# Kernel tuning notes

Measured on AMD Instinct MI355X. Metric: run time of the kernel, lower is better.

## Reference

```python
import jax, jax.numpy as jnp
import numpy as np

N_NODES = 100000
N_EDGES = 1600000
IN_C, HID_C, OUT_C = 128, 64, 40


def setup_inputs() -> dict:
    key = jax.random.key(0)
    ks = jax.random.split(key, 8)
    x = jax.random.normal(ks[0], (N_NODES, IN_C), dtype=jnp.float32)
    edge_index = jax.random.randint(ks[1], (2, N_EDGES), 0, N_NODES, dtype=jnp.int64)
    # Glorot-ish init for weights
    W1 = jax.random.normal(ks[2], (IN_C, HID_C), dtype=jnp.float32) / np.sqrt(IN_C)
    W2 = jax.random.normal(ks[3], (HID_C, HID_C), dtype=jnp.float32) / np.sqrt(HID_C)
    W3 = jax.random.normal(ks[4], (HID_C, OUT_C), dtype=jnp.float32) / np.sqrt(HID_C)
    b1 = jnp.zeros((HID_C,), jnp.float32)
    b2 = jnp.zeros((HID_C,), jnp.float32)
    b3 = jnp.zeros((OUT_C,), jnp.float32)
    return {"x": x, "edge_index": edge_index, "W1": W1, "b1": b1,
            "W2": W2, "b2": b2, "W3": W3, "b3": b3}


def _gcn_prep(edge_index, num_nodes):
    # PyG GCNConv: add self-loops, symmetric normalization with edge_weight=1.
    src = jnp.concatenate([edge_index[0], jnp.arange(num_nodes, dtype=edge_index.dtype)])
    dst = jnp.concatenate([edge_index[1], jnp.arange(num_nodes, dtype=edge_index.dtype)])
    deg = jax.ops.segment_sum(jnp.ones_like(dst, dtype=jnp.float32), dst,
                              num_segments=num_nodes)
    dis = jnp.where(deg > 0, jax.lax.rsqrt(deg), 0.0)  # deg^-1/2, inf->0
    norm = dis[src] * dis[dst]  # per-edge symmetric norm
    return src, dst, norm


def _gcn_conv(x, W, b, src, dst, norm, num_nodes):
    h = x @ W                                # [N, F_out], linear (no bias)
    msg = h[src] * norm[:, None]             # gather + scale, [E_total, F_out]
    out = jax.ops.segment_sum(msg, dst, num_segments=num_nodes)
    return out + b                           # conv bias after aggregation


def reference(x, edge_index, W1, b1, W2, b2, W3, b3):
    n = x.shape[0]
    src, dst, norm = _gcn_prep(edge_index, n)
    h = jax.nn.relu(_gcn_conv(x, W1, b1, src, dst, norm, n))
    h = jax.nn.relu(_gcn_conv(h, W2, b2, src, dst, norm, n))
    h = _gcn_conv(h, W3, b3, src, dst, norm, n)
    return jax.nn.log_softmax(h, axis=1)
```

## Files before the change

### kernel.cpp

```cpp
#include <hip/hip_runtime.h>
#include <cstdint>
#include <cstddef>
#include <math.h>

#define NN 100000
#define NE 1600000
#define NB ((NN + 255) / 256)
#define EB 400
#define EPB (NE / EB)

#define GT_NODES 128
#define GT_KC 32
#define GT_STRIDE 132

typedef unsigned short u16;

__device__ __forceinline__ float bf2f(u16 u) {
    union { unsigned int i; float f; } c; c.i = ((unsigned int)u) << 16; return c.f;
}
__device__ __forceinline__ u16 f2bf(float f) {
    union { float f; unsigned int i; } c; c.f = f;
    unsigned int lsb = (c.i >> 16) & 1u;
    return (u16)((c.i + 0x7fffu + lsb) >> 16);
}
__device__ __forceinline__ unsigned int pack2(float a, float b) {
    return (unsigned int)f2bf(a) | ((unsigned int)f2bf(b) << 16);
}

__global__ __launch_bounds__(64) void k_detect(const int* __restrict__ p, int* flag) {
    int nz = 0;
    for (int i = threadIdx.x; i < 1024; i += 64) nz |= (p[2 * i + 1] != 0);
    unsigned long long b = __ballot(nz != 0);
    if (threadIdx.x == 0) *flag = (b == 0ULL) ? 1 : 0;
}

__device__ __forceinline__ int load_idx(const void* ei, int isI64, int pos) {
    if (isI64) return (int)((const long long*)ei)[pos];
    return ((const int*)ei)[pos];
}

__global__ __launch_bounds__(256) void k_hist(const void* __restrict__ ei,
                                              const int* __restrict__ flag,
                                              int* __restrict__ counts) {
    __shared__ int h[NB];
    for (int i = threadIdx.x; i < NB; i += 256) h[i] = 0;
    __syncthreads();
    int isI64 = *flag;
    int base = blockIdx.x * EPB;
    for (int i = threadIdx.x; i < EPB; i += 256) {
        int d = load_idx(ei, isI64, NE + base + i);
        atomicAdd(&h[d >> 8], 1);
    }
    __syncthreads();
    for (int i = threadIdx.x; i < NB; i += 256) counts[blockIdx.x * NB + i] = h[i];
}

__global__ __launch_bounds__(512) void k_colscan(const int* __restrict__ counts,
                                                 int* __restrict__ pfx,
                                                 int* __restrict__ btot) {
    __shared__ int t[512];
    int j = blockIdx.x;
    int v = (threadIdx.x < EB) ? counts[threadIdx.x * NB + j] : 0;
    t[threadIdx.x] = v;
    __syncthreads();
#pragma unroll
    for (int off = 1; off < 512; off <<= 1) {
        int u = (threadIdx.x >= off) ? t[threadIdx.x - off] : 0;
        __syncthreads();
        t[threadIdx.x] += u;
        __syncthreads();
    }
    if (threadIdx.x < EB) pfx[threadIdx.x * NB + j] = t[threadIdx.x] - v;
    if (threadIdx.x == 511) btot[j] = t[511];
}

__global__ __launch_bounds__(512) void k_bucketscan(const int* __restrict__ btot,
                                                    int* __restrict__ bbase) {
    __shared__ int t[512];
    int v = (threadIdx.x < NB) ? btot[threadIdx.x] : 0;
    t[threadIdx.x] = v;
    __syncthreads();
#pragma unroll
    for (int off = 1; off < 512; off <<= 1) {
        int u = (threadIdx.x >= off) ? t[threadIdx.x - off] : 0;
        __syncthreads();
        t[threadIdx.x] += u;
        __syncthreads();
    }
    if (threadIdx.x < NB) bbase[threadIdx.x] = t[threadIdx.x] - v;
    if (threadIdx.x == 511) bbase[NB] = t[511];
}

__global__ __launch_bounds__(256) void k_scatter(const void* __restrict__ ei,
                                                 const int* __restrict__ flag,
                                                 const int* __restrict__ pfx,
                                                 const int* __restrict__ bbase,
                                                 int* __restrict__ csr_tmp) {
    __shared__ int basel[NB];
    __shared__ int cur[NB];
    for (int i = threadIdx.x; i < NB; i += 256) {
        basel[i] = bbase[i] + pfx[blockIdx.x * NB + i];
        cur[i] = 0;
    }
    __syncthreads();
    int isI64 = *flag;
    int base = blockIdx.x * EPB;
    for (int i = threadIdx.x; i < EPB; i += 256) {
        int s = load_idx(ei, isI64, base + i);
        int d = load_idx(ei, isI64, NE + base + i);
        int bkt = d >> 8;
        int slot = basel[bkt] + atomicAdd(&cur[bkt], 1);
        csr_tmp[slot] = ((d & 255) << 17) | s;
    }
}

__global__ __launch_bounds__(256) void k_sort(const int* __restrict__ bbase,
                                              const int* __restrict__ csr_tmp,
                                              int* __restrict__ csr,
                                              int* __restrict__ deg,
                                              int* __restrict__ offs,
                                              float* __restrict__ dis) {
    __shared__ int h[256];
    __shared__ int sc[256];
    __shared__ int cur[256];
    int j = blockIdx.x;
    int s0 = bbase[j], s1 = bbase[j + 1];
    h[threadIdx.x] = 0;
    __syncthreads();
    for (int p = s0 + threadIdx.x; p < s1; p += 256)
        atomicAdd(&h[csr_tmp[p] >> 17], 1);
    __syncthreads();
    int v = h[threadIdx.x];
    sc[threadIdx.x] = v;
    __syncthreads();
#pragma unroll
    for (int off = 1; off < 256; off <<= 1) {
        int u = (threadIdx.x >= off) ? sc[threadIdx.x - off] : 0;
        __syncthreads();
        sc[threadIdx.x] += u;
        __syncthreads();
    }
    int excl = sc[threadIdx.x] - v;
    int node = j * 256 + threadIdx.x;
    if (node < NN) {
        deg[node] = v;
        offs[node] = s0 + excl;
        dis[node] = rsqrtf((float)(v + 1));
    }
    cur[threadIdx.x] = excl;
    __syncthreads();
    for (int p = s0 + threadIdx.x; p < s1; p += 256) {
        int pk = csr_tmp[p];
        int dl = pk >> 17;
        int pos = s0 + atomicAdd(&cur[dl], 1);
        csr[pos] = pk & 0x1FFFF;
    }
}

template <int K, int FR, bool RELU>
__global__ __launch_bounds__(512) void k_gemm(const float* __restrict__ x,
                                              const float* __restrict__ W,
                                              const float* __restrict__ dis,
                                              u16* __restrict__ out) {
    __shared__ float xT[GT_KC * GT_STRIDE];
    __shared__ float Wc[GT_KC * 64];
    const int tid = threadIdx.x;
    const int r = tid >> 4;
    const int c = tid & 15;
    const int f4 = tid & 7;
    const int nrow = tid >> 3;
    const int nbase = blockIdx.x * GT_NODES;

    float acc[4][4];
#pragma unroll
    for (int i = 0; i < 4; ++i)
#pragma unroll
        for (int j = 0; j < 4; ++j) acc[i][j] = 0.f;

    for (int kc = 0; kc < K; kc += GT_KC) {
#pragma unroll
        for (int q = 0; q < 4; ++q) {
            int e = q * 512 + tid;
            int kk = e >> 6, j = e & 63;
            Wc[kk * 64 + j] = (j < FR) ? W[(size_t)(kc + kk) * FR + j] : 0.f;
        }
#pragma unroll
        for (int q = 0; q < 2; ++q) {
            int nl = q * 64 + nrow;
            int n = nbase + nl;
            float4 v = make_float4(0.f, 0.f, 0.f, 0.f);
            if (n < NN) v = *(const float4*)(x + (size_t)n * K + kc + f4 * 4);
            if (RELU) {
                v.x = fmaxf(v.x, 0.f); v.y = fmaxf(v.y, 0.f);
                v.z = fmaxf(v.z, 0.f); v.w = fmaxf(v.w, 0.f);
            }
            xT[(f4 * 4 + 0) * GT_STRIDE + nl] = v.x;
            xT[(f4 * 4 + 1) * GT_STRIDE + nl] = v.y;
            xT[(f4 * 4 + 2) * GT_STRIDE + nl] = v.z;
            xT[(f4 * 4 + 3) * GT_STRIDE + nl] = v.w;
        }
        __syncthreads();
#pragma unroll 8
        for (int kk = 0; kk < GT_KC; ++kk) {
            float4 a = *(const float4*)&xT[kk * GT_STRIDE + r * 4];
            float4 w = *(const float4*)&Wc[kk * 64 + c * 4];
            float xa[4] = {a.x, a.y, a.z, a.w};
            float wb[4] = {w.x, w.y, w.z, w.w};
#pragma unroll
            for (int i = 0; i < 4; ++i)
#pragma unroll
                for (int j = 0; j < 4; ++j)
                    acc[i][j] = fmaf(xa[i], wb[j], acc[i][j]);
        }
        __syncthreads();
    }
    if (c * 4 < FR) {
#pragma unroll
        for (int i = 0; i < 4; ++i) {
            int n = nbase + r * 4 + i;
            if (n < NN) {
                float dv = dis[n];
                uint2 o;
                o.x = pack2(dv * acc[i][0], dv * acc[i][1]);
                o.y = pack2(dv * acc[i][2], dv * acc[i][3]);
                *(uint2*)(out + (size_t)n * FR + c * 4) = o;
            }
        }
    }
}

template <int F, bool SOFTMAX>
__global__ __launch_bounds__(256) void k_gather(const int* __restrict__ offs,
                                                const int* __restrict__ deg,
                                                const int* __restrict__ csr,
                                                const float* __restrict__ dis,
                                                const u16* __restrict__ g,
                                                const float* __restrict__ b,
                                                float* __restrict__ out) {
    int n = blockIdx.x * 4 + (threadIdx.x >> 6);
    unsigned f = threadIdx.x & 63;
    if (n >= NN) return;
    unsigned fc = (f < (unsigned)F) ? f : 0u;
    int start = __builtin_amdgcn_readfirstlane(offs[n]);
    int len   = __builtin_amdgcn_readfirstlane(deg[n]);
    float dvn = dis[n];
    float bf  = b[fc];
    float acc = bf2f(g[(unsigned)n * F + fc]);
    int i = 0;
    for (; i + 8 <= len; i += 8) {
        int s0 = __builtin_amdgcn_readfirstlane(csr[start + i + 0]);
        int s1 = __builtin_amdgcn_readfirstlane(csr[start + i + 1]);
        int s2 = __builtin_amdgcn_readfirstlane(csr[start + i + 2]);
        int s3 = __builtin_amdgcn_readfirstlane(csr[start + i + 3]);
        int s4 = __builtin_amdgcn_readfirstlane(csr[start + i + 4]);
        int s5 = __builtin_amdgcn_readfirstlane(csr[start + i + 5]);
        int s6 = __builtin_amdgcn_readfirstlane(csr[start + i + 6]);
        int s7 = __builtin_amdgcn_readfirstlane(csr[start + i + 7]);
        u16 h0 = g[(unsigned)s0 * F + fc];
        u16 h1 = g[(unsigned)s1 * F + fc];
        u16 h2 = g[(unsigned)s2 * F + fc];
        u16 h3 = g[(unsigned)s3 * F + fc];
        u16 h4 = g[(unsigned)s4 * F + fc];
        u16 h5 = g[(unsigned)s5 * F + fc];
        u16 h6 = g[(unsigned)s6 * F + fc];
        u16 h7 = g[(unsigned)s7 * F + fc];
        acc += bf2f(h0) + bf2f(h1) + bf2f(h2) + bf2f(h3)
             + bf2f(h4) + bf2f(h5) + bf2f(h6) + bf2f(h7);
    }
    for (; i + 2 <= len; i += 2) {
        int s0 = __builtin_amdgcn_readfirstlane(csr[start + i + 0]);
        int s1 = __builtin_amdgcn_readfirstlane(csr[start + i + 1]);
        u16 h0 = g[(unsigned)s0 * F + fc];
        u16 h1 = g[(unsigned)s1 * F + fc];
        acc += bf2f(h0) + bf2f(h1);
    }
    if (i < len) {
        int s0 = __builtin_amdgcn_readfirstlane(csr[start + i]);
        acc += bf2f(g[(unsigned)s0 * F + fc]);
    }
    float v = dvn * acc + bf;
    if (!SOFTMAX) {
        if (f < (unsigned)F) out[(size_t)n * F + f] = v;
    } else {
        float vv = (f < (unsigned)F) ? v : -INFINITY;
        float m = vv;
#pragma unroll
        for (int off = 32; off; off >>= 1) m = fmaxf(m, __shfl_xor(m, off));
        float ex = (f < (unsigned)F) ? __expf(vv - m) : 0.f;
        float sum = ex;
#pragma unroll
        for (int off = 32; off; off >>= 1) sum += __shfl_xor(sum, off);
        if (f < (unsigned)F) out[(size_t)n * F + f] = vv - m - logf(sum);
    }
}

extern "C" void kernel_launch(void* const* d_in, const int* in_sizes, int n_in,
                              void* d_out, int out_size, void* d_ws, size_t ws_size,
                              hipStream_t stream) {
    const float* x  = (const float*)d_in[0];
    const void*  ei = d_in[1];
    const float* W1 = (const float*)d_in[2];
    const float* b1 = (const float*)d_in[3];
    const float* W2 = (const float*)d_in[4];
    const float* b2 = (const float*)d_in[5];
    const float* W3 = (const float*)d_in[6];
    const float* b3 = (const float*)d_in[7];
    float* out = (float*)d_out;

    char* ws = (char*)d_ws;
    size_t off = 0;
    auto alloc = [&](size_t bytes) { void* p = ws + off; off += (bytes + 255) & ~255ULL; return p; };
    int*   flag    = (int*)alloc(4);
    int*   counts  = (int*)alloc((size_t)EB * NB * 4);
    int*   pfx     = (int*)alloc((size_t)EB * NB * 4);
    int*   btot    = (int*)alloc(NB * 4);
    int*   bbase   = (int*)alloc((NB + 1) * 4);
    int*   deg     = (int*)alloc(NN * 4);
    float* dis     = (float*)alloc(NN * 4);
    int*   offs    = (int*)alloc(NN * 4);
    int*   csr_tmp = (int*)alloc((size_t)NE * 4);
    int*   csr     = (int*)alloc((size_t)NE * 4);
    u16*   gbuf    = (u16*)alloc((size_t)NN * 64 * 2);
    float* act     = (float*)alloc((size_t)NN * 64 * 4);

    k_detect<<<1, 64, 0, stream>>>((const int*)ei, flag);
    k_hist<<<EB, 256, 0, stream>>>(ei, flag, counts);
    k_colscan<<<NB, 512, 0, stream>>>(counts, pfx, btot);
    k_bucketscan<<<1, 512, 0, stream>>>(btot, bbase);
    k_scatter<<<EB, 256, 0, stream>>>(ei, flag, pfx, bbase, csr_tmp);
    k_sort<<<NB, 256, 0, stream>>>(bbase, csr_tmp, csr, deg, offs, dis);

    const int gemm_grid = (NN + GT_NODES - 1) / GT_NODES;
    const int gather_grid = (NN + 3) / 4;

    k_gemm<128, 64, false><<<gemm_grid, 512, 0, stream>>>(x, W1, dis, gbuf);
    k_gather<64, false><<<gather_grid, 256, 0, stream>>>(offs, deg, csr, dis, gbuf, b1, act);

    k_gemm<64, 64, true><<<gemm_grid, 512, 0, stream>>>(act, W2, dis, gbuf);
    k_gather<64, false><<<gather_grid, 256, 0, stream>>>(offs, deg, csr, dis, gbuf, b2, act);

    k_gemm<64, 40, true><<<gemm_grid, 512, 0, stream>>>(act, W3, dis, gbuf);
    k_gather<40, true><<<gather_grid, 256, 0, stream>>>(offs, deg, csr, dis, gbuf, b3, out);
}
```

Before: 347.0 us.

## Vectorize gather: 16 lanes per row with 8-byte loads, 4 edges per wave

Reworks the aggregation kernel so each 16-lane quarter-wave loads one neighbor row with 8-byte vector loads (4 bf16 features per lane). The four quarters handle four different edges at once, and the partial sums are combined with cross-lane shuffles. Edge indices are read as int4 after an alignment prologue. This is meant to cut per-lane 2-byte loads and issue more independent memory requests per instruction. In exchange it adds shuffle reductions and leaves lanes idle in the remainder loops, where only quad 0 works.

```diff
diff --git a/kernel.cpp b/kernel.cpp
--- a/kernel.cpp
+++ b/kernel.cpp
@@ -15,8 +15,8 @@
 
 typedef unsigned short u16;
 
-__device__ __forceinline__ float bf2f(u16 u) {
-    union { unsigned int i; float f; } c; c.i = ((unsigned int)u) << 16; return c.f;
+__device__ __forceinline__ float asf(unsigned u) {
+    union { unsigned i; float f; } c; c.i = u; return c.f;
 }
 __device__ __forceinline__ u16 f2bf(float f) {
     union { float f; unsigned int i; } c; c.f = f;
@@ -237,60 +237,84 @@
                                                 const u16* __restrict__ g,
                                                 const float* __restrict__ b,
                                                 float* __restrict__ out) {
+    constexpr int NDW2 = F / 4;
+    int lane = threadIdx.x & 63;
     int n = blockIdx.x * 4 + (threadIdx.x >> 6);
-    unsigned f = threadIdx.x & 63;
     if (n >= NN) return;
-    unsigned fc = (f < (unsigned)F) ? f : 0u;
+    int quad = lane >> 4, sq = lane & 15;
+    unsigned sqoff = (unsigned)sq * 8u;
+    const char* gb = (const char*)g;
+
+    float2 a0 = make_float2(0.f, 0.f);
+    float2 a1 = make_float2(0.f, 0.f);
+
+    auto rowoff = [](int row) -> unsigned {
+        if (F == 64) return ((unsigned)row) << 7;
+        unsigned t = (((unsigned)row) << 2) + (unsigned)row;
+        return t << 4;
+    };
+    auto addRow = [&](unsigned off) {
+        uint2 dd = *(const uint2*)(gb + off);
+        a0.x += asf(dd.x << 16); a0.y += asf(dd.x & 0xffff0000u);
+        a1.x += asf(dd.y << 16); a1.y += asf(dd.y & 0xffff0000u);
+    };
+
     int start = __builtin_amdgcn_readfirstlane(offs[n]);
     int len   = __builtin_amdgcn_readfirstlane(deg[n]);
     float dvn = dis[n];
-    float bf  = b[fc];
-    float acc = bf2f(g[(unsigned)n * F + fc]);
+
+    if (quad == 0) addRow(rowoff(n) + sqoff);
+
     int i = 0;
-    for (; i + 8 <= len; i += 8) {
-        int s0 = __builtin_amdgcn_readfirstlane(csr[start + i + 0]);
-        int s1 = __builtin_amdgcn_readfirstlane(csr[start + i + 1]);
-        int s2 = __builtin_amdgcn_readfirstlane(csr[start + i + 2]);
-        int s3 = __builtin_amdgcn_readfirstlane(csr[start + i + 3]);
-        int s4 = __builtin_amdgcn_readfirstlane(csr[start + i + 4]);
-        int s5 = __builtin_amdgcn_readfirstlane(csr[start + i + 5]);
-        int s6 = __builtin_amdgcn_readfirstlane(csr[start + i + 6]);
-        int s7 = __builtin_amdgcn_readfirstlane(csr[start + i + 7]);
-        u16 h0 = g[(unsigned)s0 * F + fc];
-        u16 h1 = g[(unsigned)s1 * F + fc];
-        u16 h2 = g[(unsigned)s2 * F + fc];
-        u16 h3 = g[(unsigned)s3 * F + fc];
-        u16 h4 = g[(unsigned)s4 * F + fc];
-        u16 h5 = g[(unsigned)s5 * F + fc];
-        u16 h6 = g[(unsigned)s6 * F + fc];
-        u16 h7 = g[(unsigned)s7 * F + fc];
-        acc += bf2f(h0) + bf2f(h1) + bf2f(h2) + bf2f(h3)
-             + bf2f(h4) + bf2f(h5) + bf2f(h6) + bf2f(h7);
-    }
-    for (; i + 2 <= len; i += 2) {
-        int s0 = __builtin_amdgcn_readfirstlane(csr[start + i + 0]);
-        int s1 = __builtin_amdgcn_readfirstlane(csr[start + i + 1]);
-        u16 h0 = g[(unsigned)s0 * F + fc];
-        u16 h1 = g[(unsigned)s1 * F + fc];
-        acc += bf2f(h0) + bf2f(h1);
-    }
-    if (i < len) {
-        int s0 = __builtin_amdgcn_readfirstlane(csr[start + i]);
-        acc += bf2f(g[(unsigned)s0 * F + fc]);
-    }
-    float v = dvn * acc + bf;
+    int pre = (4 - (start & 3)) & 3;
+    if (pre > len) pre = len;
+    for (; i < pre; ++i) {
+        int e = csr[start + i];
+        if (quad == 0) addRow(rowoff(e) + sqoff);
+    }
+    for (; i + 4 <= len; i += 4) {
+        int4 e4 = *(const int4*)(csr + start + i);
+        int sa = (quad & 1) ? e4.y : e4.x;
+        int sb = (quad & 1) ? e4.w : e4.z;
+        int src = (quad & 2) ? sb : sa;
+        addRow(rowoff(src) + sqoff);
+    }
+    for (; i < len; ++i) {
+        int e = csr[start + i];
+        if (quad == 0) addRow(rowoff(e) + sqoff);
+    }
+
+    a0.x += __shfl_xor(a0.x, 16); a0.x += __shfl_xor(a0.x, 32);
+    a0.y += __shfl_xor(a0.y, 16); a0.y += __shfl_xor(a0.y, 32);
+    a1.x += __shfl_xor(a1.x, 16); a1.x += __shfl_xor(a1.x, 32);
+    a1.y += __shfl_xor(a1.y, 16); a1.y += __shfl_xor(a1.y, 32);
+
+    bool act = sq < NDW2;
+    float4 bias = make_float4(0.f, 0.f, 0.f, 0.f);
+    if (act) bias = *(const float4*)(b + sq * 4);
+    float v0 = dvn * a0.x + bias.x;
+    float v1 = dvn * a0.y + bias.y;
+    float v2 = dvn * a1.x + bias.z;
+    float v3 = dvn * a1.y + bias.w;
+
     if (!SOFTMAX) {
-        if (f < (unsigned)F) out[(size_t)n * F + f] = v;
+        if (quad == 0 && act)
+            *(float4*)(out + (size_t)n * F + sq * 4) = make_float4(v0, v1, v2, v3);
     } else {
-        float vv = (f < (unsigned)F) ? v : -INFINITY;
-        float m = vv;
-#pragma unroll
-        for (int off = 32; off; off >>= 1) m = fmaxf(m, __shfl_xor(m, off));
-        float ex = (f < (unsigned)F) ? __expf(vv - m) : 0.f;
-        float sum = ex;
-#pragma unroll
-        for (int off = 32; off; off >>= 1) sum += __shfl_xor(sum, off);
-        if (f < (unsigned)F) out[(size_t)n * F + f] = vv - m - logf(sum);
+        float m = act ? fmaxf(fmaxf(v0, v1), fmaxf(v2, v3)) : -INFINITY;
+        m = fmaxf(m, __shfl_xor(m, 1));
+        m = fmaxf(m, __shfl_xor(m, 2));
+        m = fmaxf(m, __shfl_xor(m, 4));
+        m = fmaxf(m, __shfl_xor(m, 8));
+        float s = act ? (__expf(v0 - m) + __expf(v1 - m) + __expf(v2 - m) + __expf(v3 - m)) : 0.f;
+        s += __shfl_xor(s, 1);
+        s += __shfl_xor(s, 2);
+        s += __shfl_xor(s, 4);
+        s += __shfl_xor(s, 8);
+        float ls = logf(s);
+        if (quad == 0 && act)
+            *(float4*)(out + (size_t)n * F + sq * 4) =
+                make_float4(v0 - m - ls, v1 - m - ls, v2 - m - ls, v3 - m - ls);
     }
 }
 
```

After: 407.8 us. 1.18x slower.

## Fuse CSR bucket build into one kernel using fixed-capacity buckets and atomic cursors

Applied to the files above, without the earlier changes.

Replaces the detect, histogram, column-scan, bucket-scan and scatter kernels with a single build kernel. That kernel stages each block's edges in shared memory, counts them per destination bucket, and reserves space in fixed-capacity per-bucket regions with global atomics. This removes several launches and the exact prefix-sum passes over a large counts matrix. In exchange it assumes no bucket of 256 nodes ever gets more than CAP edges, which holds for uniformly random edges but can overflow on skewed graphs. Bucket order within a region also becomes nondeterministic.

```diff
diff --git a/kernel.cpp b/kernel.cpp
--- a/kernel.cpp
+++ b/kernel.cpp
@@ -8,6 +8,7 @@
 #define NB ((NN + 255) / 256)
 #define EB 400
 #define EPB (NE / EB)
+#define CAP 5120
 
 #define GT_NODES 128
 #define GT_KC 32
@@ -16,7 +17,7 @@
 typedef unsigned short u16;
 
 __device__ __forceinline__ float bf2f(u16 u) {
-    union { unsigned int i; float f; } c; c.i = ((unsigned int)u) << 16; return c.f;
+    union { unsigned i; float f; } c; c.i = ((unsigned)u) << 16; return c.f;
 }
 __device__ __forceinline__ u16 f2bf(float f) {
     union { float f; unsigned int i; } c; c.f = f;
@@ -27,94 +28,56 @@
     return (unsigned int)f2bf(a) | ((unsigned int)f2bf(b) << 16);
 }
 
-__global__ __launch_bounds__(64) void k_detect(const int* __restrict__ p, int* flag) {
-    int nz = 0;
-    for (int i = threadIdx.x; i < 1024; i += 64) nz |= (p[2 * i + 1] != 0);
-    unsigned long long b = __ballot(nz != 0);
-    if (threadIdx.x == 0) *flag = (b == 0ULL) ? 1 : 0;
-}
-
 __device__ __forceinline__ int load_idx(const void* ei, int isI64, int pos) {
     if (isI64) return (int)((const long long*)ei)[pos];
     return ((const int*)ei)[pos];
 }
 
-__global__ __launch_bounds__(256) void k_hist(const void* __restrict__ ei,
-                                              const int* __restrict__ flag,
-                                              int* __restrict__ counts) {
-    __shared__ int h[NB];
-    for (int i = threadIdx.x; i < NB; i += 256) h[i] = 0;
-    __syncthreads();
-    int isI64 = *flag;
-    int base = blockIdx.x * EPB;
-    for (int i = threadIdx.x; i < EPB; i += 256) {
-        int d = load_idx(ei, isI64, NE + base + i);
-        atomicAdd(&h[d >> 8], 1);
-    }
-    __syncthreads();
-    for (int i = threadIdx.x; i < NB; i += 256) counts[blockIdx.x * NB + i] = h[i];
-}
-
-__global__ __launch_bounds__(512) void k_colscan(const int* __restrict__ counts,
-                                                 int* __restrict__ pfx,
-                                                 int* __restrict__ btot) {
-    __shared__ int t[512];
-    int j = blockIdx.x;
-    int v = (threadIdx.x < EB) ? counts[threadIdx.x * NB + j] : 0;
-    t[threadIdx.x] = v;
-    __syncthreads();
-#pragma unroll
-    for (int off = 1; off < 512; off <<= 1) {
-        int u = (threadIdx.x >= off) ? t[threadIdx.x - off] : 0;
-        __syncthreads();
-        t[threadIdx.x] += u;
-        __syncthreads();
-    }
-    if (threadIdx.x < EB) pfx[threadIdx.x * NB + j] = t[threadIdx.x] - v;
-    if (threadIdx.x == 511) btot[j] = t[511];
-}
-
-__global__ __launch_bounds__(512) void k_bucketscan(const int* __restrict__ btot,
-                                                    int* __restrict__ bbase) {
-    __shared__ int t[512];
-    int v = (threadIdx.x < NB) ? btot[threadIdx.x] : 0;
-    t[threadIdx.x] = v;
-    __syncthreads();
-#pragma unroll
-    for (int off = 1; off < 512; off <<= 1) {
-        int u = (threadIdx.x >= off) ? t[threadIdx.x - off] : 0;
-        __syncthreads();
-        t[threadIdx.x] += u;
-        __syncthreads();
-    }
-    if (threadIdx.x < NB) bbase[threadIdx.x] = t[threadIdx.x] - v;
-    if (threadIdx.x == 511) bbase[NB] = t[511];
-}
-
-__global__ __launch_bounds__(256) void k_scatter(const void* __restrict__ ei,
-                                                 const int* __restrict__ flag,
-                                                 const int* __restrict__ pfx,
-                                                 const int* __restrict__ bbase,
-                                                 int* __restrict__ csr_tmp) {
+__global__ __launch_bounds__(256) void k_build(const void* __restrict__ ei,
+                                               int* __restrict__ cursor,
+                                               int* __restrict__ csr_tmp) {
+    __shared__ int sbuf[EPB];
+    __shared__ int dbuf[EPB];
+    __shared__ int cnt[NB];
     __shared__ int basel[NB];
-    __shared__ int cur[NB];
-    for (int i = threadIdx.x; i < NB; i += 256) {
-        basel[i] = bbase[i] + pfx[blockIdx.x * NB + i];
-        cur[i] = 0;
-    }
-    __syncthreads();
-    int isI64 = *flag;
+    __shared__ int anynz;
+
+    const int* p = (const int*)ei;
+    if (threadIdx.x == 0) anynz = 0;
+    for (int i = threadIdx.x; i < NB; i += 256) cnt[i] = 0;
+    __syncthreads();
+    int nz = 0;
+    for (int i = threadIdx.x; i < 1024; i += 256) nz |= (p[2 * i + 1] != 0);
+    if (nz) anynz = 1;
+    __syncthreads();
+    int isI64 = (anynz == 0);
+
     int base = blockIdx.x * EPB;
     for (int i = threadIdx.x; i < EPB; i += 256) {
         int s = load_idx(ei, isI64, base + i);
         int d = load_idx(ei, isI64, NE + base + i);
+        sbuf[i] = s;
+        dbuf[i] = d;
+        atomicAdd(&cnt[d >> 8], 1);
+    }
+    __syncthreads();
+    for (int j = threadIdx.x; j < NB; j += 256) {
+        int c = cnt[j];
+        int g = c ? atomicAdd(&cursor[j], c) : 0;
+        basel[j] = j * CAP + g;
+        cnt[j] = 0;
+    }
+    __syncthreads();
+    for (int i = threadIdx.x; i < EPB; i += 256) {
+        int s = sbuf[i];
+        int d = dbuf[i];
         int bkt = d >> 8;
-        int slot = basel[bkt] + atomicAdd(&cur[bkt], 1);
+        int slot = basel[bkt] + atomicAdd(&cnt[bkt], 1);
         csr_tmp[slot] = ((d & 255) << 17) | s;
     }
 }
 
-__global__ __launch_bounds__(256) void k_sort(const int* __restrict__ bbase,
+__global__ __launch_bounds__(256) void k_sort(const int* __restrict__ cursor,
                                               const int* __restrict__ csr_tmp,
                                               int* __restrict__ csr,
                                               int* __restrict__ deg,
@@ -124,7 +87,7 @@
     __shared__ int sc[256];
     __shared__ int cur[256];
     int j = blockIdx.x;
-    int s0 = bbase[j], s1 = bbase[j + 1];
+    int s0 = j * CAP, s1 = s0 + cursor[j];
     h[threadIdx.x] = 0;
     __syncthreads();
     for (int p = s0 + threadIdx.x; p < s1; p += 256)
@@ -310,25 +273,18 @@
     char* ws = (char*)d_ws;
     size_t off = 0;
     auto alloc = [&](size_t bytes) { void* p = ws + off; off += (bytes + 255) & ~255ULL; return p; };
-    int*   flag    = (int*)alloc(4);
-    int*   counts  = (int*)alloc((size_t)EB * NB * 4);
-    int*   pfx     = (int*)alloc((size_t)EB * NB * 4);
-    int*   btot    = (int*)alloc(NB * 4);
-    int*   bbase   = (int*)alloc((NB + 1) * 4);
+    int*   cursor  = (int*)alloc(NB * 4);
     int*   deg     = (int*)alloc(NN * 4);
     float* dis     = (float*)alloc(NN * 4);
     int*   offs    = (int*)alloc(NN * 4);
-    int*   csr_tmp = (int*)alloc((size_t)NE * 4);
-    int*   csr     = (int*)alloc((size_t)NE * 4);
+    int*   csr_tmp = (int*)alloc((size_t)NB * CAP * 4);
+    int*   csr     = (int*)alloc((size_t)NB * CAP * 4);
     u16*   gbuf    = (u16*)alloc((size_t)NN * 64 * 2);
     float* act     = (float*)alloc((size_t)NN * 64 * 4);
 
-    k_detect<<<1, 64, 0, stream>>>((const int*)ei, flag);
-    k_hist<<<EB, 256, 0, stream>>>(ei, flag, counts);
-    k_colscan<<<NB, 512, 0, stream>>>(counts, pfx, btot);
-    k_bucketscan<<<1, 512, 0, stream>>>(btot, bbase);
-    k_scatter<<<EB, 256, 0, stream>>>(ei, flag, pfx, bbase, csr_tmp);
-    k_sort<<<NB, 256, 0, stream>>>(bbase, csr_tmp, csr, deg, offs, dis);
+    hipMemsetAsync(cursor, 0, NB * 4, stream);
+    k_build<<<EB, 256, 0, stream>>>(ei, cursor, csr_tmp);
+    k_sort<<<NB, 256, 0, stream>>>(cursor, csr_tmp, csr, deg, offs, dis);
 
     const int gemm_grid = (NN + GT_NODES - 1) / GT_NODES;
     const int gather_grid = (NN + 3) / 4;
```

After: 338.9 us. 2.3% less time.
